# Optimization experiments

Measured on AMD Instinct MI355X. Metric: run time of the kernel, lower is better.

The kernel has to match this reference:

```python
import jax, jax.numpy as jnp
import numpy as np

# dims from VideoTokenizerConfig defaults + chosen video shape
B, T, IH, IW, C = 2, 16, 224, 224, 3
TP, PS, D, DFF, L, NH, K = 4, 16, 512, 2048, 6, 8, 8192
Tp, Hp, Wp = T // TP, IH // PS, IW // PS   # 4, 14, 14
S = Tp * Hp * Wp                           # 784 tokens
PIN = TP * PS * PS * C                     # 3072 patch elements
COMMIT = 0.25


def _ln(x, s, b):
    m = x.mean(-1, keepdims=True)
    v = ((x - m) ** 2).mean(-1, keepdims=True)
    return (x - m) / jnp.sqrt(v + 1e-6) * s + b


def _mha(x, Wqkv, bqkv, Wo, bo):
    b_, s_, d_ = x.shape
    hd = d_ // NH
    q = (x @ Wqkv[0] + bqkv[0]).reshape(b_, s_, NH, hd)
    k = (x @ Wqkv[1] + bqkv[1]).reshape(b_, s_, NH, hd)
    v = (x @ Wqkv[2] + bqkv[2]).reshape(b_, s_, NH, hd)
    att = jax.nn.softmax(jnp.einsum('bqhd,bkhd->bhqk', q, k) / jnp.sqrt(jnp.float32(hd)), axis=-1)
    o = jnp.einsum('bhqk,bkhd->bqhd', att, v).reshape(b_, s_, d_)
    return o @ Wo + bo


def _blocks(z, ln1s, ln1b, Wqkv, bqkv, Wo, bo, ln2s, ln2b, W1, b1, W2, b2):
    for i in range(L):  # small fixed layer count
        z = z + _mha(_ln(z, ln1s[i], ln1b[i]), Wqkv[i], bqkv[i], Wo[i], bo[i])
        h = jax.nn.gelu(_ln(z, ln2s[i], ln2b[i]) @ W1[i] + b1[i])
        z = z + h @ W2[i] + b2[i]
    return z


def _forward(video, e_patch_W, e_patch_b, e_pos_t, e_pos_h, e_pos_w,
             e_ln1_s, e_ln1_b, e_Wqkv, e_bqkv, e_Wo, e_bo, e_ln2_s, e_ln2_b,
             e_W1, e_b1, e_W2, e_b2, e_lnf_s, e_lnf_b, e_cb_W, e_cb_b,
             codebook,
             d_cb_W, d_cb_b, d_pos_t, d_pos_h, d_pos_w,
             d_ln1_s, d_ln1_b, d_Wqkv, d_bqkv, d_Wo, d_bo, d_ln2_s, d_ln2_b,
             d_W1, d_b1, d_W2, d_b2, d_lnf_s, d_lnf_b, d_px_W, d_px_b):
    # ---- encoder: 3D patchify ----
    v = video.reshape(B, Tp, TP, Hp, PS, Wp, PS, C)
    v = v.transpose(0, 1, 3, 5, 2, 4, 6, 7).reshape(B, Tp, Hp, Wp, PIN)
    z = v @ e_patch_W + e_patch_b
    z = z + e_pos_t + e_pos_h + e_pos_w
    z = z.reshape(B, S, D)
    z = _blocks(z, e_ln1_s, e_ln1_b, e_Wqkv, e_bqkv, e_Wo, e_bo,
                e_ln2_s, e_ln2_b, e_W1, e_b1, e_W2, e_b2)
    z = _ln(z, e_lnf_s, e_lnf_b)
    z_e = z @ e_cb_W + e_cb_b                      # [B,S,D]
    # ---- VQ quantize ----
    flat = z_e.reshape(-1, D)                      # [B*S, D]
    d2 = (flat ** 2).sum(1, keepdims=True) + (codebook ** 2).sum(1) - 2.0 * flat @ codebook.T
    idx = jnp.argmin(d2, axis=1)                   # [B*S]
    z_q = codebook[idx].reshape(z_e.shape)
    commit = jnp.mean((jax.lax.stop_gradient(z_q) - z_e) ** 2)
    cb_loss = jnp.mean((z_q - jax.lax.stop_gradient(z_e)) ** 2)
    z_q = z_e + jax.lax.stop_gradient(z_q - z_e)   # straight-through
    counts = jnp.zeros((K,), flat.dtype).at[idx].add(1.0)
    p = counts / idx.shape[0]                      # == mean(one_hot, axis=0)
    perplexity = jnp.exp(-jnp.sum(p * jnp.log(p + 1e-10)))
    # ---- decoder ----
    zd = z_q.reshape(B, Tp, Hp, Wp, D) @ d_cb_W + d_cb_b
    zd = zd + d_pos_t + d_pos_h + d_pos_w
    zd = zd.reshape(B, S, D)
    zd = _blocks(zd, d_ln1_s, d_ln1_b, d_Wqkv, d_bqkv, d_Wo, d_bo,
                 d_ln2_s, d_ln2_b, d_W1, d_b1, d_W2, d_b2)
    zd = _ln(zd, d_lnf_s, d_lnf_b)
    px = zd.reshape(B, Tp, Hp, Wp, D) @ d_px_W + d_px_b
    px = px.reshape(B, Tp, Hp, Wp, TP, PS, PS, C)
    recon = px.transpose(0, 1, 4, 2, 5, 3, 6, 7).reshape(B, T, IH, IW, C)
    return recon, idx.reshape(B, Tp, Hp, Wp), commit, cb_loss, perplexity


def setup_inputs() -> dict:
    key = jax.random.key(0)
    ks = iter(jax.random.split(key, 48))
    def nrm(shape, s=0.02):
        return (s * jax.random.normal(next(ks), shape)).astype(jnp.float32)
    z = lambda shape: jnp.zeros(shape, jnp.float32)
    o = lambda shape: jnp.ones(shape, jnp.float32)
    inp = {}
    inp['video'] = jax.random.normal(next(ks), (B, T, IH, IW, C), jnp.float32)
    # encoder params
    inp['e_patch_W'] = nrm((PIN, D)); inp['e_patch_b'] = z((D,))
    inp['e_pos_t'] = nrm((1, Tp, 1, 1, D)); inp['e_pos_h'] = nrm((1, 1, Hp, 1, D)); inp['e_pos_w'] = nrm((1, 1, 1, Wp, D))
    inp['e_ln1_s'] = o((L, D)); inp['e_ln1_b'] = z((L, D))
    inp['e_Wqkv'] = nrm((L, 3, D, D)); inp['e_bqkv'] = z((L, 3, D))
    inp['e_Wo'] = nrm((L, D, D)); inp['e_bo'] = z((L, D))
    inp['e_ln2_s'] = o((L, D)); inp['e_ln2_b'] = z((L, D))
    inp['e_W1'] = nrm((L, D, DFF)); inp['e_b1'] = z((L, DFF))
    inp['e_W2'] = nrm((L, DFF, D)); inp['e_b2'] = z((L, D))
    inp['e_lnf_s'] = o((D,)); inp['e_lnf_b'] = z((D,))
    inp['e_cb_W'] = nrm((D, D)); inp['e_cb_b'] = z((D,))
    inp['codebook'] = nrm((K, D))
    # decoder params
    inp['d_cb_W'] = nrm((D, D)); inp['d_cb_b'] = z((D,))
    inp['d_pos_t'] = nrm((1, Tp, 1, 1, D)); inp['d_pos_h'] = nrm((1, 1, Hp, 1, D)); inp['d_pos_w'] = nrm((1, 1, 1, Wp, D))
    inp['d_ln1_s'] = o((L, D)); inp['d_ln1_b'] = z((L, D))
    inp['d_Wqkv'] = nrm((L, 3, D, D)); inp['d_bqkv'] = z((L, 3, D))
    inp['d_Wo'] = nrm((L, D, D)); inp['d_bo'] = z((L, D))
    inp['d_ln2_s'] = o((L, D)); inp['d_ln2_b'] = z((L, D))
    inp['d_W1'] = nrm((L, D, DFF)); inp['d_b1'] = z((L, DFF))
    inp['d_W2'] = nrm((L, DFF, D)); inp['d_b2'] = z((L, D))
    inp['d_lnf_s'] = o((D,)); inp['d_lnf_b'] = z((D,))
    inp['d_px_W'] = nrm((D, PIN)); inp['d_px_b'] = z((PIN,))
    return inp


def reference(video, e_patch_W, e_patch_b, e_pos_t, e_pos_h, e_pos_w,
              e_ln1_s, e_ln1_b, e_Wqkv, e_bqkv, e_Wo, e_bo, e_ln2_s, e_ln2_b,
              e_W1, e_b1, e_W2, e_b2, e_lnf_s, e_lnf_b, e_cb_W, e_cb_b,
              codebook,
              d_cb_W, d_cb_b, d_pos_t, d_pos_h, d_pos_w,
              d_ln1_s, d_ln1_b, d_Wqkv, d_bqkv, d_Wo, d_bo, d_ln2_s, d_ln2_b,
              d_W1, d_b1, d_W2, d_b2, d_lnf_s, d_lnf_b, d_px_W, d_px_b):
    return _forward(video, e_patch_W, e_patch_b, e_pos_t, e_pos_h, e_pos_w,
                    e_ln1_s, e_ln1_b, e_Wqkv, e_bqkv, e_Wo, e_bo, e_ln2_s, e_ln2_b,
                    e_W1, e_b1, e_W2, e_b2, e_lnf_s, e_lnf_b, e_cb_W, e_cb_b,
                    codebook,
                    d_cb_W, d_cb_b, d_pos_t, d_pos_h, d_pos_w,
                    d_ln1_s, d_ln1_b, d_Wqkv, d_bqkv, d_Wo, d_bo, d_ln2_s, d_ln2_b,
                    d_W1, d_b1, d_W2, d_b2, d_lnf_s, d_lnf_b, d_px_W, d_px_b)
```

## Files before the change

### kernel.cpp

```cpp
#include <hip/hip_runtime.h>
#include <math.h>

#define Bq    2
#define Dq    512
#define DFFq  2048
#define Lq    6
#define NHq   8
#define HDq   64
#define Kq    8192
#define Sq    784
#define PINq  3072
#define TOKq  1568
#define RECN  4816896L

#define OFF_BIG  0L
#define SZ_BIG   12845056L
#define OFF_Z    (OFF_BIG + SZ_BIG)
#define OFF_XLN  (OFF_Z    + 802816L)
#define OFF_QKV  (OFF_XLN  + 802816L)
#define OFF_ATTO (OFF_QKV  + 2408448L)
#define OFF_H    (OFF_ATTO + 802816L)
#define OFF_ZE   (OFF_H    + 3211264L)
#define OFF_ZQ   (OFF_ZE   + 802816L)
#define OFF_CN   (OFF_ZQ   + 802816L)
#define OFF_IDX  (OFF_CN   + 8192L)
#define OFF_CNT  (OFF_IDX  + 1568L)
#define OFF_PART (OFF_CNT  + 8192L)
#define OFF_MIN  (OFF_PART + 1568L)
#define OFF_END  (OFF_MIN  + 3136L)

#define CEXT 802816L

typedef short bf16x8 __attribute__((ext_vector_type(8)));
typedef float f32x4  __attribute__((ext_vector_type(4)));
typedef unsigned short u16;
typedef unsigned long long u64;

#define XLO 802816L
#define QLO 2408448L
#define ALO 802816L
#define HLO 3211264L
#define PLO 4816896L
#define ZLO 802816L
#define CBLO 4194304L


__device__ __forceinline__ float wave_sum(float v) {
    #pragma unroll
    for (int o = 32; o; o >>= 1) v += __shfl_xor(v, o);
    return v;
}
__device__ __forceinline__ float gelu_f(float x) {
    float u = 0.7978845608028654f * (x + 0.044715f * x * x * x);
    float a = fabsf(u);
    float t = __expf(-2.0f * a);
    float th = (1.0f - t) / (1.0f + t);
    th = copysignf(th, u);
    return 0.5f * x * (1.0f + th);
}
__device__ __forceinline__ void split_f32(float x, u16& h, u16& l) {
    unsigned u = __float_as_uint(x);
    unsigned t = u + 0x7fffu + ((u >> 16) & 1u);
    h = (u16)(t >> 16);
    float r = x - __uint_as_float((t >> 16) << 16);
    l = (u16)(__float_as_uint(r) >> 16);
}
__device__ __forceinline__ void gload16(const u16* g, u16* l) {
    __builtin_amdgcn_global_load_lds(
        (const __attribute__((address_space(1))) void*)g,
        (__attribute__((address_space(3))) void*)l,
        16, 0, 0);
}

__global__ __launch_bounds__(256)
void wconv_t(const float* __restrict__ W, int ldw, int Kd,
             u16* __restrict__ WT, long loT, long soW, long soT)
{
    __shared__ u16 Lh[32][33], Ll[32][33];
    const float* Wp = W + (long)blockIdx.z * soW;
    u16* Tp = WT + (long)blockIdx.z * soT;
    int k0 = blockIdx.x << 5, n0 = blockIdx.y << 5;
    int t = threadIdx.x;
    int r = t >> 3, c4 = (t & 7) << 2;
    float4 v = *(const float4*)(Wp + (long)(k0 + r) * ldw + n0 + c4);
    u16 h, l;
    split_f32(v.x, h, l); Lh[c4+0][r] = h; Ll[c4+0][r] = l;
    split_f32(v.y, h, l); Lh[c4+1][r] = h; Ll[c4+1][r] = l;
    split_f32(v.z, h, l); Lh[c4+2][r] = h; Ll[c4+2][r] = l;
    split_f32(v.w, h, l); Lh[c4+3][r] = h; Ll[c4+3][r] = l;
    __syncthreads();
    int n = t >> 3, kc = (t & 7) << 2;
    u16* dst = Tp + (long)(n0 + n) * Kd + k0 + kc;
    u16 oh[4] = {Lh[n][kc], Lh[n][kc+1], Lh[n][kc+2], Lh[n][kc+3]};
    u16 ol[4] = {Ll[n][kc], Ll[n][kc+1], Ll[n][kc+2], Ll[n][kc+3]};
    *(uint2*)dst = *(uint2*)oh;
    *(uint2*)(dst + loT) = *(uint2*)ol;
}

// ... 13 lines not shown
    } else if (id < 1024) {
        int rid = id - 768; kblk = rid & 15; nblk = rid >> 4;
        W = Wo; ldw = 512; Kd = 512; Tp = dst + 1572864; loT = 262144;
    } else if (id < 2048) {
        int rid = id - 1024; kblk = rid & 15; nblk = rid >> 4;
        W = W1; ldw = 2048; Kd = 512; Tp = dst + 2097152; loT = 1048576;
    } else {
        int rid = id - 2048; kblk = rid & 63; nblk = rid >> 6;
        W = W2; ldw = 512; Kd = 2048; Tp = dst + 4194304; loT = 1048576;
    }
    int k0 = kblk << 5, n0 = nblk << 5;
    int t = threadIdx.x;
    int r = t >> 3, c4 = (t & 7) << 2;
    float4 v = *(const float4*)(W + (long)(k0 + r) * ldw + n0 + c4);
    u16 h, l;
    split_f32(v.x, h, l); Lh[c4+0][r] = h; Ll[c4+0][r] = l;
    split_f32(v.y, h, l); Lh[c4+1][r] = h; Ll[c4+1][r] = l;
    split_f32(v.z, h, l); Lh[c4+2][r] = h; Ll[c4+2][r] = l;
    split_f32(v.w, h, l); Lh[c4+3][r] = h; Ll[c4+3][r] = l;
    __syncthreads();
    int n = t >> 3, kc = (t & 7) << 2;
    u16* d = Tp + (long)(n0 + n) * Kd + k0 + kc;
    u16 oh[4] = {Lh[n][kc], Lh[n][kc+1], Lh[n][kc+2], Lh[n][kc+3]};
    u16 ol[4] = {Ll[n][kc], Ll[n][kc+1], Ll[n][kc+2], Ll[n][kc+3]};
    *(uint2*)d = *(uint2*)oh;
    *(uint2*)(d + loT) = *(uint2*)ol;
}

__global__ __launch_bounds__(256)
void splitp(const float* __restrict__ X, u16* __restrict__ Y, long lo, long n4)
{
    long i = (long)blockIdx.x * 256 + threadIdx.x;
    if (i >= n4) return;
    float4 v = *(const float4*)(X + i * 4);
    u16 h[4], l[4];
    split_f32(v.x, h[0], l[0]); split_f32(v.y, h[1], l[1]);
    split_f32(v.z, h[2], l[2]); split_f32(v.w, h[3], l[3]);
    *(uint2*)(Y + i * 4) = *(uint2*)h;
    *(uint2*)(Y + lo + i * 4) = *(uint2*)l;
}

template<int MATH, bool X2>
__global__ __launch_bounds__(256)
void gemm_bb(const u16* __restrict__ A, long rsA, long loA, long soA, long siA,
             const u16* __restrict__ B, long rsB, long loB, long soB, long siB,
             const float* __restrict__ bias, long siBias,
             const float* __restrict__ extra,
             float* __restrict__ Cf, int ldc, long soC, long siC,
             u16* __restrict__ Cb, int rsC, long loC,
             float* __restrict__ part, long pstride,
             int M, int N, int K, float alpha,
             int bdiv, int ksplit, int klen, int gx)
{
    __shared__ u16 Ah[2][2048], Al[2][2048], Bh[2][2048], Bl[2][2048];
    const int zb2 = blockIdx.z;
    const int zk = zb2 % ksplit, zb = zb2 / ksplit;
    const int zo = zb / bdiv, zi = zb - zo * bdiv;
    A += zo * soA + zi * siA;
    B += zo * soB + zi * siB;
    const float* bi = bias ? bias + zi * siBias : nullptr;

    const int nwg = gridDim.x;
    int orig = blockIdx.x;
    int qq = nwg >> 3, rr = nwg & 7;
    int xcd = orig & 7, sidx = orig >> 3;
    int wgid = (xcd < rr ? xcd * (qq + 1) : rr * (qq + 1) + (xcd - rr) * qq) + sidx;
    const int m0 = (wgid % gx) << 6, n0 = (wgid / gx) << 6;

    const int t = threadIdx.x;
    const int kbeg = zk * klen;
    int kend = kbeg + klen; if (kend > K) kend = K;

    const int w = t >> 6, lane = t & 63;
    const int wm = w >> 1, wn = w & 1;
    const int l15 = lane & 15, lk = (lane >> 4) << 3;
    const int wq = w << 9;

    int arow = m0 + (t >> 2); if (arow > M - 1) arow = M - 1;
    const u16* Apr = A + (long)arow * rsA + ((t & 3) << 3);
    const u16* Bpr = B + (long)(n0 + (t >> 2)) * rsB + ((t & 3) << 3);

    f32x4 acc[2][2] = {};

    for (int k0 = kbeg; k0 < kend; k0 += 64) {
        gload16(Apr + k0,            &Ah[0][wq]);
        gload16(Apr + k0 + loA,      &Al[0][wq]);
        gload16(Bpr + k0,            &Bh[0][wq]);
        if (!X2) gload16(Bpr + k0 + loB, &Bl[0][wq]);
        gload16(Apr + k0 + 32,       &Ah[1][wq]);
        gload16(Apr + k0 + 32 + loA, &Al[1][wq]);
        gload16(Bpr + k0 + 32,       &Bh[1][wq]);
        if (!X2) gload16(Bpr + k0 + 32 + loB, &Bl[1][wq]);
        __syncthreads();

        #pragma unroll
        for (int sub = 0; sub < 2; ++sub) {
            bf16x8 ah[2], al2[2], bh2[2], bl2[2];
            #pragma unroll
            for (int mi = 0; mi < 2; ++mi) {
                int row = (wm << 5) + (mi << 4) + l15;
                ah[mi]  = *(const bf16x8*)&Ah[sub][(row << 5) + lk];
                al2[mi] = *(const bf16x8*)&Al[sub][(row << 5) + lk];
            }
            #pragma unroll
            for (int ni = 0; ni < 2; ++ni) {
                int row = (wn << 5) + (ni << 4) + l15;
                bh2[ni] = *(const bf16x8*)&Bh[sub][(row << 5) + lk];
                if (!X2) bl2[ni] = *(const bf16x8*)&Bl[sub][(row << 5) + lk];
            }
            #pragma unroll
            for (int mi = 0; mi < 2; ++mi)
                #pragma unroll
                for (int ni = 0; ni < 2; ++ni) {
                    acc[mi][ni] = __builtin_amdgcn_mfma_f32_16x16x32_bf16(ah[mi], bh2[ni], acc[mi][ni], 0, 0, 0);
                    if (!X2) acc[mi][ni] = __builtin_amdgcn_mfma_f32_16x16x32_bf16(ah[mi], bl2[ni], acc[mi][ni], 0, 0, 0);
                    acc[mi][ni] = __builtin_amdgcn_mfma_f32_16x16x32_bf16(al2[mi], bh2[ni], acc[mi][ni], 0, 0, 0);
                }
        }
        __syncthreads();
    }

    if (ksplit > 1) {
        float* P = part + (long)zk * pstride + zo * soC + zi * siC;
        #pragma unroll
        for (int mi = 0; mi < 2; ++mi)
            #pragma unroll
            for (int ni = 0; ni < 2; ++ni) {
                int gn = n0 + (wn << 5) + (ni << 4) + l15;
                if (gn >= N) continue;
                int gmb = m0 + (wm << 5) + (mi << 4) + ((lane >> 4) << 2);
                #pragma unroll
                for (int r = 0; r < 4; ++r) {
                    int gm = gmb + r;
                    if (gm < M) P[(long)gm * ldc + gn] = acc[mi][ni][r];
                }
            }
        return;
    }
    if (MATH == 0) {
        float* Co = Cf + zo * soC + zi * siC;
        #pragma unroll
        for (int mi = 0; mi < 2; ++mi)
            #pragma unroll
            for (int ni = 0; ni < 2; ++ni) {
                int gn = n0 + (wn << 5) + (ni << 4) + l15;
                if (gn >= N) continue;
                int gmb = m0 + (wm << 5) + (mi << 4) + ((lane >> 4) << 2);
                #pragma unroll
                for (int r = 0; r < 4; ++r) {
                    int gm = gmb + r;
                    if (gm >= M) continue;
                    Co[(long)gm * ldc + gn] = alpha * acc[mi][ni][r] + (bi ? bi[gn] : 0.0f);
                }
            }
    } else if (MATH == 5) {
        u64* mb = (u64*)Cf;
        #pragma unroll
        for (int mi = 0; mi < 2; ++mi) {
            #pragma unroll
            for (int r = 0; r < 4; ++r) {
                u64 best = 0xFFFFFFFFFFFFFFFFULL;
                #pragma unroll
                for (int ni = 0; ni < 2; ++ni) {
                    int gn = n0 + (wn << 5) + (ni << 4) + l15;
                    float v = extra[gn] - 2.0f * acc[mi][ni][r];
                    unsigned ub = __float_as_uint(v);
                    ub = ub ^ ((ub >> 31) ? 0xFFFFFFFFu : 0x80000000u);
                    u64 pk = ((u64)ub << 32) | (unsigned)gn;
                    best = pk < best ? pk : best;
                }
                #pragma unroll
                for (int sft = 1; sft <= 8; sft <<= 1) {
                    u64 o = __shfl_xor(best, sft);
                    best = o < best ? o : best;
                }
                if (l15 == 0) {
                    int gm = m0 + (wm << 5) + (mi << 4) + ((lane >> 4) << 2) + r;
                    if (gm < M) atomicMin(&mb[gm], best);
                }
            }
        }
    } else {
        u16* Cu = Cb + zo * soC + zi * siC;
        #pragma unroll
        for (int mi = 0; mi < 2; ++mi)
            #pragma unroll
            for (int ni = 0; ni < 2; ++ni) {
                int gn = n0 + (wn << 5) + (ni << 4) + l15;
                if (gn >= N) continue;
                int gmb = m0 + (wm << 5) + (mi << 4) + ((lane >> 4) << 2);
                #pragma unroll
                for (int r = 0; r < 4; ++r) {
                    int gm = gmb + r;
                    if (gm >= M) continue;
                    float v = acc[mi][ni][r] + bi[gn];
                    u16 h, l; split_f32(v, h, l);
                    Cu[(long)gm * rsC + gn] = h;
                    Cu[(long)gm * rsC + gn + loC] = l;
                }
            }
    }
}

#define KP 72
#define VP 40
#define CHR 196
template<bool X2>
__global__ __launch_bounds__(256)
void flash_kernel(const u16* __restrict__ qkv, float* __restrict__ O4, float* __restrict__ ML)
{
    __shared__ u16 Kh[32 * KP], Kl[32 * KP];
    __shared__ u16 Vh[64 * VP], Vl[64 * VP];
    __shared__ u16 Ph[64 * VP], Pl[64 * VP];

    const int qb = blockIdx.x, bh = blockIdx.y, ch = blockIdx.z;
    const int b = bh >> 3, h = bh & 7;
    const int jbeg = ch * CHR, jend = jbeg + CHR;
    const int t = threadIdx.x, w = t >> 6, lane = t & 63;
    const int l15 = lane & 15, g = lane >> 4;
    const long base = (long)b * 784 * 1536;
    const u16* Qg = qkv + base + h * 64;
    const u16* Kg = qkv + base + 512 + h * 64;
    const u16* Vg = qkv + base + 1024 + h * 64;

    const int q0 = qb << 6;
    int qr = q0 + w * 16 + l15; if (qr > 783) qr = 783;
    const u16* Qp = Qg + (long)qr * 1536 + g * 8;
    bf16x8 qh[2], ql[2];
    qh[0] = *(const bf16x8*)(Qp);
    qh[1] = *(const bf16x8*)(Qp + 32);
    ql[0] = *(const bf16x8*)(Qp + QLO);
    ql[1] = *(const bf16x8*)(Qp + QLO + 32);

    f32x4 O[4] = {};
    float m_[4] = {-1e30f, -1e30f, -1e30f, -1e30f};
    float l_[4] = {};

    const int srow = t >> 3, sc = (t & 7) << 3;

    for (int j0 = jbeg; j0 < jend; j0 += 32) {
        {
            int jr = j0 + srow;
            if (jr < jend) {
                const u16* Kp = Kg + (long)jr * 1536 + sc;
                *(uint4*)&Kh[srow * KP + sc] = *(const uint4*)(Kp);
                if (!X2) *(uint4*)&Kl[srow * KP + sc] = *(const uint4*)(Kp + QLO);
                const u16* Vp = Vg + (long)jr * 1536 + sc;
                u16 th[8], tl[8];
                *(uint4*)th = *(const uint4*)Vp;
                if (!X2) *(uint4*)tl = *(const uint4*)(Vp + QLO);
                #pragma unroll
                for (int e = 0; e < 8; ++e) {
                    Vh[(sc + e) * VP + srow] = th[e];
                    if (!X2) Vl[(sc + e) * VP + srow] = tl[e];
                }
            } else {
                uint4 zz = {0, 0, 0, 0};
                *(uint4*)&Kh[srow * KP + sc] = zz;
                if (!X2) *(uint4*)&Kl[srow * KP + sc] = zz;
                #pragma unroll
                for (int e = 0; e < 8; ++e) {
                    Vh[(sc + e) * VP + srow] = 0;
                    if (!X2) Vl[(sc + e) * VP + srow] = 0;
                }
            }
        }
        __syncthreads();

        f32x4 S[2] = {};
        #pragma unroll
        for (int f = 0; f < 2; ++f) {
            #pragma unroll
            for (int ks = 0; ks < 2; ++ks) {
                bf16x8 kh = *(const bf16x8*)&Kh[(f * 16 + l15) * KP + ks * 32 + g * 8];
                S[f] = __builtin_amdgcn_mfma_f32_16x16x32_bf16(qh[ks], kh, S[f], 0, 0, 0);
                if (!X2) {
                    bf16x8 kl = *(const bf16x8*)&Kl[(f * 16 + l15) * KP + ks * 32 + g * 8];
                    S[f] = __builtin_amdgcn_mfma_f32_16x16x32_bf16(qh[ks], kl, S[f], 0, 0, 0);
                }
                S[f] = __builtin_amdgcn_mfma_f32_16x16x32_bf16(ql[ks], kh, S[f], 0, 0, 0);
            }
        }

        float p[2][4];
        #pragma unroll
        for (int f = 0; f < 2; ++f) {
            bool ok = (j0 + f * 16 + l15) < jend;
            #pragma unroll
            for (int r = 0; r < 4; ++r)
                p[f][r] = ok ? S[f][r] * 0.125f : -1e30f;
        }
        #pragma unroll
        for (int r = 0; r < 4; ++r) {
            float pm = fmaxf(p[0][r], p[1][r]);
            pm = fmaxf(pm, __shfl_xor(pm, 1)); pm = fmaxf(pm, __shfl_xor(pm, 2));
            pm = fmaxf(pm, __shfl_xor(pm, 4)); pm = fmaxf(pm, __shfl_xor(pm, 8));
            float mn = fmaxf(m_[r], pm);
            float scl = __expf(m_[r] - mn);
            float rs = 0.f;
            #pragma unroll
            for (int f = 0; f < 2; ++f) { float e = __expf(p[f][r] - mn); p[f][r] = e; rs += e; }
            rs += __shfl_xor(rs, 1); rs += __shfl_xor(rs, 2);
            rs += __shfl_xor(rs, 4); rs += __shfl_xor(rs, 8);
            l_[r] = l_[r] * scl + rs;
            m_[r] = mn;
            O[0][r] *= scl; O[1][r] *= scl; O[2][r] *= scl; O[3][r] *= scl;
        }

        #pragma unroll
        for (int f = 0; f < 2; ++f)
            #pragma unroll
            for (int r = 0; r < 4; ++r) {
                u16 hh, ll; split_f32(p[f][r], hh, ll);
                int row = w * 16 + g * 4 + r;
                Ph[row * VP + f * 16 + l15] = hh;
                Pl[row * VP + f * 16 + l15] = ll;
            }

        bf16x8 pah = *(const bf16x8*)&Ph[(w * 16 + l15) * VP + g * 8];
        bf16x8 pal = *(const bf16x8*)&Pl[(w * 16 + l15) * VP + g * 8];
        #pragma unroll
        for (int f = 0; f < 4; ++f) {
            bf16x8 vh = *(const bf16x8*)&Vh[(f * 16 + l15) * VP + g * 8];
            O[f] = __builtin_amdgcn_mfma_f32_16x16x32_bf16(pah, vh, O[f], 0, 0, 0);
            O[f] = __builtin_amdgcn_mfma_f32_16x16x32_bf16(pal, vh, O[f], 0, 0, 0);
            if (!X2) {
                bf16x8 vl = *(const bf16x8*)&Vl[(f * 16 + l15) * VP + g * 8];
                O[f] = __builtin_amdgcn_mfma_f32_16x16x32_bf16(pah, vl, O[f], 0, 0, 0);
            }
        }
        __syncthreads();
    }

    #pragma unroll
    for (int r = 0; r < 4; ++r) {
        int q = q0 + w * 16 + g * 4 + r;
        if (q >= 784) continue;
        long rowi = ((long)ch * 16 + bh) * 784 + q;
        if (l15 == 0) { ML[rowi * 2] = m_[r]; ML[rowi * 2 + 1] = l_[r]; }
        #pragma unroll
        for (int f = 0; f < 4; ++f)
            O4[rowi * 64 + f * 16 + l15] = O[f][r];
    }
}

__global__ __launch_bounds__(256)
void flash_combine(const float* __restrict__ O4, const float* __restrict__ ML,
                   u16* __restrict__ atto)
{
    int wave = threadIdx.x >> 6, lane = threadIdx.x & 63;
    int row = (blockIdx.x << 2) + wave;
    int bh = row / 784, q = row - bh * 784;
    int b = bh >> 3, h = bh & 7;
    float mm[4], ll[4];
    float M = -1e30f;
    #pragma unroll
    for (int c = 0; c < 4; ++c) {
        long ri = ((long)c * 16 + bh) * 784 + q;
        mm[c] = ML[ri * 2]; ll[c] = ML[ri * 2 + 1];
        M = fmaxf(M, mm[c]);
    }
    float L = 0.f, sc[4];
    #pragma unroll
    for (int c = 0; c < 4; ++c) { sc[c] = __expf(mm[c] - M); L += sc[c] * ll[c]; }
    float o = 0.f;
    #pragma unroll
    for (int c = 0; c < 4; ++c)
        o += O4[(((long)c * 16 + bh) * 784 + q) * 64 + lane] * sc[c];
    o /= L;
    u16 hh, lo2; split_f32(o, hh, lo2);
    long off = ((long)b * 784 + q) * 512 + h * 64 + lane;
    atto[off] = hh; atto[off + ALO] = lo2;
}

template<int MATH>
__global__ __launch_bounds__(256)
void reduce_k(const float* __restrict__ part, long pstride, int ks,
              const float* __restrict__ bias, int ldc,
              float* __restrict__ Cf, u16* __restrict__ Cb, long loC, long total)
{
    long i = (long)blockIdx.x * 256 + threadIdx.x;
    if (i >= total) return;
    float s = 0.f;
    for (int k = 0; k < ks; ++k) s += part[(long)k * pstride + i];
    int col = (int)(i % ldc);
    float v = s + (bias ? bias[col] : 0.0f);
    if (MATH == 3) { Cf[i] = v; u16 h, l; split_f32(v, h, l); Cb[i] = h; Cb[i + loC] = l; }
    else { float g = gelu_f(v); u16 h, l; split_f32(g, h, l); Cb[i] = h; Cb[i + loC] = l; }
}

__global__ __launch_bounds__(256)
void redln(const float* __restrict__ part, long pstride, int ks,
           const float* __restrict__ bias,
           float* __restrict__ z,
           const float* __restrict__ s, const float* __restrict__ b,
           u16* __restrict__ y, long lo)
{
    int wave = threadIdx.x >> 6, lane = threadIdx.x & 63;
    int row = (blockIdx.x << 2) + wave;
    int c0 = lane << 3;
    long base = (long)row * 512 + c0;
    float a[8] = {};
    for (int k = 0; k < ks; ++k) {
        const float* p = part + (long)k * pstride + base;
        float4 p0 = *(const float4*)p, p1 = *(const float4*)(p + 4);
        a[0]+=p0.x; a[1]+=p0.y; a[2]+=p0.z; a[3]+=p0.w;
        a[4]+=p1.x; a[5]+=p1.y; a[6]+=p1.z; a[7]+=p1.w;
    }
    float4 b0 = *(const float4*)(bias + c0), b1 = *(const float4*)(bias + c0 + 4);
    a[0]+=b0.x; a[1]+=b0.y; a[2]+=b0.z; a[3]+=b0.w;
    a[4]+=b1.x; a[5]+=b1.y; a[6]+=b1.z; a[7]+=b1.w;
    float4 z0 = *(const float4*)(z + base), z1 = *(const float4*)(z + base + 4);
    float v[8] = { z0.x+a[0], z0.y+a[1], z0.z+a[2], z0.w+a[3],
                   z1.x+a[4], z1.y+a[5], z1.z+a[6], z1.w+a[7] };
    float4 o0, o1;
    o0.x=v[0]; o0.y=v[1]; o0.z=v[2]; o0.w=v[3];
    o1.x=v[4]; o1.y=v[5]; o1.z=v[6]; o1.w=v[7];
    *(float4*)(z + base) = o0; *(float4*)(z + base + 4) = o1;
    float sum = v[0]+v[1]+v[2]+v[3]+v[4]+v[5]+v[6]+v[7];
    sum = wave_sum(sum);
    float m = sum * (1.0f / 512.0f);
    float var = 0.f;
    float d[8];
    #pragma unroll
    for (int j = 0; j < 8; ++j) { d[j] = v[j] - m; var += d[j]*d[j]; }
    var = wave_sum(var);
    float rstd = 1.0f / sqrtf(var * (1.0f / 512.0f) + 1e-6f);
    u16 hh[8], ll[8];
    #pragma unroll
    for (int j = 0; j < 8; ++j)
        split_f32(d[j] * rstd * s[c0+j] + b[c0+j], hh[j], ll[j]);
    *(uint4*)(y + base) = *(uint4*)hh;
    *(uint4*)(y + lo + base) = *(uint4*)ll;
}

__global__ __launch_bounds__(256)
void redposln(const float* __restrict__ part, long pstride, int ks,
              const float* __restrict__ bias,
              const float* __restrict__ pt, const float* __restrict__ ph,
              const float* __restrict__ pw,
// ... 104 lines not shown
        u16 h, l; split_f32(cv, h, l);
        zqp[(long)tok * Dq + d] = h;
        zqp[lo + (long)tok * Dq + d] = l;
        float df = cv - z[d];
        ss += df * df;
    }
    float wsum = wave_sum(ss);
    __shared__ float sw[4];
    if ((threadIdx.x & 63) == 0) sw[threadIdx.x >> 6] = wsum;
    __syncthreads();
    if (threadIdx.x == 0) {
        part[tok] = sw[0] + sw[1] + sw[2] + sw[3];
        atomicAdd(&counts[id], 1.0f);
        out_idx[tok] = (float)id;
    }
}

__global__ __launch_bounds__(256)
void scalars_kernel(const float* __restrict__ part, const float* __restrict__ counts,
                    float* __restrict__ out)
{
    float se = 0.f;
    for (int t = threadIdx.x; t < TOKq; t += 256) se += part[t];
    float pl = 0.f;
    for (int k = threadIdx.x; k < Kq; k += 256) {
        float p = counts[k] * (1.0f / 1568.0f);
        pl += p * logf(p + 1e-10f);
    }
    float wse = wave_sum(se), wpl = wave_sum(pl);
    __shared__ float s1[4], s2[4];
    if ((threadIdx.x & 63) == 0) { s1[threadIdx.x >> 6] = wse; s2[threadIdx.x >> 6] = wpl; }
    __syncthreads();
    if (threadIdx.x == 0) {
        float sse = s1[0] + s1[1] + s1[2] + s1[3];
        float plo = s2[0] + s2[1] + s2[2] + s2[3];
        float commit = sse / 802816.0f;
        out[RECN + 1568 + 0] = commit;
        out[RECN + 1568 + 1] = commit;
        out[RECN + 1568 + 2] = expf(-plo);
    }
}

template<bool X2>
static void block_fwd(hipStream_t st, float* z, float* big, float* hbuf,
                      u16* xlnu, u16* qkvu, u16* attou, u16* hbu, u16* wscr,
                      const float* Wqkv, const float* bqkv,
                      const float* Wo, const float* bo,
                      const float* ln2s, const float* ln2b,
                      const float* W1, const float* b1,
                      const float* W2, const float* b2,
                      const float* nls, const float* nlb)
{
    wconv4<<<3072, 256, 0, st>>>(Wqkv, Wo, W1, W2, wscr);
    gemm_bb<4, X2><<<dim3(600, 1, 1), 256, 0, st>>>(
        xlnu, Dq, XLO, 0, 0,
        wscr, Dq, 786432, 0, 0,
        bqkv, 0, nullptr,
        nullptr, 0, 0, 0,
        qkvu, 1536, QLO,
        nullptr, 0,
        TOKq, 1536, Dq, 1.0f, 1, 1, Dq, 25);
    flash_kernel<X2><<<dim3(13, 16, 4), 256, 0, st>>>(qkvu, big, big + 3211264L);
    flash_combine<<<3136, 256, 0, st>>>(big, big + 3211264L, attou);
    gemm_bb<0, X2><<<dim3(200, 1, 4), 256, 0, st>>>(
        attou, Dq, ALO, 0, 0,
        wscr + 1572864, Dq, 262144, 0, 0,
        nullptr, 0, nullptr,
        nullptr, Dq, 0, 0,
        nullptr, 0, 0,
        hbuf, CEXT,
        TOKq, Dq, Dq, 1.0f, 1, 4, 128, 25);
    redln<<<392, 256, 0, st>>>(hbuf, CEXT, 4, bo, z, ln2s, ln2b, xlnu, XLO);
    gemm_bb<0, X2><<<dim3(800, 1, 2), 256, 0, st>>>(
        xlnu, Dq, XLO, 0, 0,
        wscr + 2097152, Dq, 1048576, 0, 0,
        nullptr, 0, nullptr,
        nullptr, DFFq, 0, 0,
        nullptr, 0, 0,
        big, 3211264L,
        TOKq, DFFq, Dq, 1.0f, 1, 2, 256, 25);
    reduce_k<4><<<(3211264L + 255) / 256, 256, 0, st>>>(big, 3211264L, 2, b1, DFFq, nullptr, hbu, HLO, 3211264L);
    gemm_bb<0, X2><<<dim3(200, 1, 4), 256, 0, st>>>(
        hbu, DFFq, HLO, 0, 0,
        wscr + 4194304, DFFq, 1048576, 0, 0,
        nullptr, 0, nullptr,
        nullptr, Dq, 0, 0,
        nullptr, 0, 0,
        big, CEXT,
        TOKq, Dq, DFFq, 1.0f, 1, 4, 512, 25);
    redln<<<392, 256, 0, st>>>(big, CEXT, 4, b2, z, nls, nlb, xlnu, XLO);
}

extern "C" void kernel_launch(void* const* d_in, const int* in_sizes, int n_in,
                              void* d_out, int out_size, void* d_ws, size_t ws_size,
                              hipStream_t stream)
{
    (void)in_sizes; (void)n_in; (void)out_size;
    if (ws_size < (size_t)OFF_END * sizeof(float)) return;

    const float* video = (const float*)d_in[0];
    const float* epW   = (const float*)d_in[1];  const float* epb   = (const float*)d_in[2];
    const float* ept   = (const float*)d_in[3];  const float* ephp  = (const float*)d_in[4];
    const float* epwp  = (const float*)d_in[5];
    const float* eln1s = (const float*)d_in[6];  const float* eln1b = (const float*)d_in[7];
    const float* eWqkv = (const float*)d_in[8];  const float* ebqkv = (const float*)d_in[9];
    const float* eWo   = (const float*)d_in[10]; const float* ebo   = (const float*)d_in[11];
    const float* eln2s = (const float*)d_in[12]; const float* eln2b = (const float*)d_in[13];
    const float* eW1   = (const float*)d_in[14]; const float* eb1   = (const float*)d_in[15];
    const float* eW2   = (const float*)d_in[16]; const float* eb2   = (const float*)d_in[17];
    const float* elnfs = (const float*)d_in[18]; const float* elnfb = (const float*)d_in[19];
    const float* ecbW  = (const float*)d_in[20]; const float* ecbb  = (const float*)d_in[21];
    const float* cbook = (const float*)d_in[22];
    const float* dcbW  = (const float*)d_in[23]; const float* dcbb  = (const float*)d_in[24];
    const float* dpt   = (const float*)d_in[25]; const float* dphp  = (const float*)d_in[26];
    const float* dpwp  = (const float*)d_in[27];
    const float* dln1s = (const float*)d_in[28]; const float* dln1b = (const float*)d_in[29];
    const float* dWqkv = (const float*)d_in[30]; const float* dbqkv = (const float*)d_in[31];
    const float* dWo   = (const float*)d_in[32]; const float* dbo   = (const float*)d_in[33];
    const float* dln2s = (const float*)d_in[34]; const float* dln2b = (const float*)d_in[35];
    const float* dW1   = (const float*)d_in[36]; const float* db1   = (const float*)d_in[37];
    const float* dW2   = (const float*)d_in[38]; const float* db2   = (const float*)d_in[39];
    const float* dlnfs = (const float*)d_in[40]; const float* dlnfb = (const float*)d_in[41];
    const float* dpxW  = (const float*)d_in[42]; const float* dpxb  = (const float*)d_in[43];

    float* ws   = (float*)d_ws;
    float* big  = ws + OFF_BIG;
    float* z    = ws + OFF_Z;
    float* xln  = ws + OFF_XLN;
    float* qkv  = ws + OFF_QKV;
    float* atto = ws + OFF_ATTO;
    float* hbuf = ws + OFF_H;
    float* ze   = ws + OFF_ZE;
    float* zq   = ws + OFF_ZQ;
    float* cn   = ws + OFF_CN;
    float* cnt  = ws + OFF_CNT;
    float* part = ws + OFF_PART;
    u64*   minb = (u64*)(ws + OFF_MIN);
    float* out  = (float*)d_out;

    u16* xlnu  = (u16*)xln;
    u16* qkvu  = (u16*)qkv;
    u16* attou = (u16*)atto;
    u16* hbu   = (u16*)hbuf;
    u16* patu  = (u16*)big;
    u16* zqu   = (u16*)zq;
    u16* cbs   = (u16*)qkv;
    u16* wscr  = (u16*)(big + 9633792);

    hipMemsetAsync(cnt, 0, Kq * sizeof(float), stream);
    hipMemsetAsync(minb, 0xFF, TOKq * sizeof(u64), stream);
    cnorm_kernel<<<Kq / 4, 256, 0, stream>>>(cbook, cn);

    patchify_kernel<<<(int)(((long)TOKq * PINq + 255) / 256), 256, 0, stream>>>(video, patu);
    wconv_t<<<dim3(96, 16, 1), 256, 0, stream>>>(epW, Dq, PINq, wscr, 1572864, 0, 0);
    gemm_bb<0, false><<<dim3(200, 1, 6), 256, 0, stream>>>(
        patu, PINq, PLO, 0, 0,
        wscr, PINq, 1572864, 0, 0,
        nullptr, 0, nullptr,
        nullptr, Dq, 0, 0,
        nullptr, 0, 0,
        big + PLO, CEXT,
        TOKq, Dq, PINq, 1.0f, 1, 6, 512, 25);
    redposln<<<392, 256, 0, stream>>>(big + PLO, CEXT, 6, epb, ept, ephp, epwp,
                                      z, eln1s, eln1b, xlnu, XLO);

    for (int l = 0; l < Lq; ++l) {
        const float* nls = (l < 5) ? eln1s + (l + 1) * Dq : elnfs;
        const float* nlb = (l < 5) ? eln1b + (l + 1) * Dq : elnfb;
        block_fwd<false>(stream, z, big, hbuf, xlnu, qkvu, attou, hbu, wscr,
                         eWqkv + (long)l * 3 * Dq * Dq, ebqkv + l * 3 * Dq,
                         eWo + (long)l * Dq * Dq, ebo + l * Dq,
                         eln2s + l * Dq, eln2b + l * Dq,
                         eW1 + (long)l * Dq * DFFq, eb1 + l * DFFq,
                         eW2 + (long)l * DFFq * Dq, eb2 + l * Dq,
                         nls, nlb);
    }

    wconv_t<<<dim3(16, 16, 1), 256, 0, stream>>>(ecbW, Dq, Dq, wscr, 262144, 0, 0);
    gemm_bb<0, false><<<dim3(200, 1, 2), 256, 0, stream>>>(
        xlnu, Dq, XLO, 0, 0,
        wscr, Dq, 262144, 0, 0,
        nullptr, 0, nullptr,
        nullptr, Dq, 0, 0,
        nullptr, 0, 0,
        big, CEXT,
        TOKq, Dq, Dq, 1.0f, 1, 2, 256, 25);
    reduce_k<3><<<(CEXT + 255) / 256, 256, 0, stream>>>(big, CEXT, 2, ecbb, Dq, ze, zqu, ZLO, CEXT);

    splitp<<<(int)(((long)Kq * Dq / 4 + 255) / 256), 256, 0, stream>>>(cbook, cbs, CBLO, (long)Kq * Dq / 4);
    gemm_bb<5, false><<<dim3(3200, 1, 1), 256, 0, stream>>>(
        zqu, Dq, ZLO, 0, 0,
        cbs, Dq, CBLO, 0, 0,
        nullptr, 0, cn,
        (float*)minb, Kq, 0, 0,
        nullptr, 0, 0,
        nullptr, 0,
        TOKq, Kq, Dq, 1.0f, 1, 1, Dq, 25);
    zq_kernel<<<TOKq, 256, 0, stream>>>(cbook, minb, ze, zqu, ZLO, part, cnt, out + RECN);
    scalars_kernel<<<1, 256, 0, stream>>>(part, cnt, out);

    wconv_t<<<dim3(16, 16, 1), 256, 0, stream>>>(dcbW, Dq, Dq, wscr, 262144, 0, 0);
    gemm_bb<0, true><<<dim3(200, 1, 2), 256, 0, stream>>>(
        zqu, Dq, ZLO, 0, 0,
        wscr, Dq, 262144, 0, 0,
        nullptr, 0, nullptr,
        nullptr, Dq, 0, 0,
        nullptr, 0, 0,
        big, CEXT,
        TOKq, Dq, Dq, 1.0f, 1, 2, 256, 25);
    redposln<<<392, 256, 0, stream>>>(big, CEXT, 2, dcbb, dpt, dphp, dpwp,
                                      z, dln1s, dln1b, xlnu, XLO);

    for (int l = 0; l < Lq; ++l) {
        const float* nls = (l < 5) ? dln1s + (l + 1) * Dq : dlnfs;
        const float* nlb = (l < 5) ? dln1b + (l + 1) * Dq : dlnfb;
        block_fwd<true>(stream, z, big, hbuf, xlnu, qkvu, attou, hbu, wscr,
                        dWqkv + (long)l * 3 * Dq * Dq, dbqkv + l * 3 * Dq,
                        dWo + (long)l * Dq * Dq, dbo + l * Dq,
                        dln2s + l * Dq, dln2b + l * Dq,
                        dW1 + (long)l * Dq * DFFq, db1 + l * DFFq,
                        dW2 + (long)l * DFFq * Dq, db2 + l * Dq,
                        nls, nlb);
    }

    wconv_t<<<dim3(16, 96, 1), 256, 0, stream>>>(dpxW, PINq, Dq, wscr, 1572864, 0, 0);
    gemm_bb<0, true><<<dim3(1200, 1, 1), 256, 0, stream>>>(
        xlnu, Dq, XLO, 0, 0,
        wscr, Dq, 1572864, 0, 0,
        dpxb, 0, nullptr,
        big, PINq, 0, 0,
        nullptr, 0, 0,
        nullptr, 0,
        TOKq, PINq, Dq, 1.0f, 1, 1, Dq, 25);
    unpatchify_kernel<<<(int)((RECN + 255) / 256), 256, 0, stream>>>(big, out);
}
```

Before: 1.839 ms.

## Size shared memory per X2 variant and raise split-K/attention chunking

GEMM and flash kernels now use a single shared array sized by the X2 template, so the bf16x2 (X2) variants reserve less LDS and can fit more blocks per CU. Attention splits keys into 8 chunks instead of 4, and the combine step merges 8 partials. The QKV GEMM becomes split-K with a separate bias-reduce pass (new MATH==2), and several other GEMMs double their K-split. This raises parallelism on small GEMMs at the cost of extra partial-sum traffic and more reduction work.

```diff
diff --git a/kernel.cpp b/kernel.cpp
--- a/kernel.cpp
+++ b/kernel.cpp
@@ -43,7 +43,6 @@
 #define PLO 4816896L
 #define ZLO 802816L
 #define CBLO 4194304L
-
 
 __device__ __forceinline__ float wave_sum(float v) {
     #pragma unroll
@@ -163,7 +162,7 @@
              int M, int N, int K, float alpha,
              int bdiv, int ksplit, int klen, int gx)
 {
-    __shared__ u16 Ah[2][2048], Al[2][2048], Bh[2][2048], Bl[2][2048];
+    __shared__ u16 SH[X2 ? 12288 : 16384];
     const int zb2 = blockIdx.z;
     const int zk = zb2 % ksplit, zb = zb2 / ksplit;
     const int zo = zb / bdiv, zi = zb - zo * bdiv;
@@ -194,30 +193,31 @@
     f32x4 acc[2][2] = {};
 
     for (int k0 = kbeg; k0 < kend; k0 += 64) {
-        gload16(Apr + k0,            &Ah[0][wq]);
-        gload16(Apr + k0 + loA,      &Al[0][wq]);
-        gload16(Bpr + k0,            &Bh[0][wq]);
-        if (!X2) gload16(Bpr + k0 + loB, &Bl[0][wq]);
-        gload16(Apr + k0 + 32,       &Ah[1][wq]);
-        gload16(Apr + k0 + 32 + loA, &Al[1][wq]);
-        gload16(Bpr + k0 + 32,       &Bh[1][wq]);
-        if (!X2) gload16(Bpr + k0 + 32 + loB, &Bl[1][wq]);
+        gload16(Apr + k0,            &SH[wq]);
+        gload16(Apr + k0 + loA,      &SH[4096 + wq]);
+        gload16(Bpr + k0,            &SH[8192 + wq]);
+        if (!X2) gload16(Bpr + k0 + loB, &SH[12288 + wq]);
+        gload16(Apr + k0 + 32,       &SH[2048 + wq]);
+        gload16(Apr + k0 + 32 + loA, &SH[4096 + 2048 + wq]);
+        gload16(Bpr + k0 + 32,       &SH[8192 + 2048 + wq]);
+        if (!X2) gload16(Bpr + k0 + 32 + loB, &SH[12288 + 2048 + wq]);
         __syncthreads();
 
         #pragma unroll
         for (int sub = 0; sub < 2; ++sub) {
+            const int so = sub << 11;
             bf16x8 ah[2], al2[2], bh2[2], bl2[2];
             #pragma unroll
             for (int mi = 0; mi < 2; ++mi) {
                 int row = (wm << 5) + (mi << 4) + l15;
-                ah[mi]  = *(const bf16x8*)&Ah[sub][(row << 5) + lk];
-                al2[mi] = *(const bf16x8*)&Al[sub][(row << 5) + lk];
+                ah[mi]  = *(const bf16x8*)&SH[so + (row << 5) + lk];
+                al2[mi] = *(const bf16x8*)&SH[4096 + so + (row << 5) + lk];
             }
             #pragma unroll
             for (int ni = 0; ni < 2; ++ni) {
                 int row = (wn << 5) + (ni << 4) + l15;
-                bh2[ni] = *(const bf16x8*)&Bh[sub][(row << 5) + lk];
-                if (!X2) bl2[ni] = *(const bf16x8*)&Bl[sub][(row << 5) + lk];
+                bh2[ni] = *(const bf16x8*)&SH[8192 + so + (row << 5) + lk];
+                if (!X2) bl2[ni] = *(const bf16x8*)&SH[12288 + so + (row << 5) + lk];
             }
             #pragma unroll
             for (int mi = 0; mi < 2; ++mi)
@@ -315,14 +315,12 @@
 
 #define KP 72
 #define VP 40
-#define CHR 196
+#define CHR 98
 template<bool X2>
 __global__ __launch_bounds__(256)
 void flash_kernel(const u16* __restrict__ qkv, float* __restrict__ O4, float* __restrict__ ML)
 {
-    __shared__ u16 Kh[32 * KP], Kl[32 * KP];
-    __shared__ u16 Vh[64 * VP], Vl[64 * VP];
-    __shared__ u16 Ph[64 * VP], Pl[64 * VP];
+    __shared__ u16 SH[X2 ? 9984 : 14848];
 
     const int qb = blockIdx.x, bh = blockIdx.y, ch = blockIdx.z;
     const int b = bh >> 3, h = bh & 7;
@@ -354,25 +352,25 @@
             int jr = j0 + srow;
             if (jr < jend) {
                 const u16* Kp = Kg + (long)jr * 1536 + sc;
-                *(uint4*)&Kh[srow * KP + sc] = *(const uint4*)(Kp);
-                if (!X2) *(uint4*)&Kl[srow * KP + sc] = *(const uint4*)(Kp + QLO);
+                *(uint4*)&SH[srow * KP + sc] = *(const uint4*)(Kp);
+                if (!X2) *(uint4*)&SH[9984 + srow * KP + sc] = *(const uint4*)(Kp + QLO);
                 const u16* Vp = Vg + (long)jr * 1536 + sc;
                 u16 th[8], tl[8];
                 *(uint4*)th = *(const uint4*)Vp;
                 if (!X2) *(uint4*)tl = *(const uint4*)(Vp + QLO);
                 #pragma unroll
                 for (int e = 0; e < 8; ++e) {
-                    Vh[(sc + e) * VP + srow] = th[e];
-                    if (!X2) Vl[(sc + e) * VP + srow] = tl[e];
+                    SH[2304 + (sc + e) * VP + srow] = th[e];
+                    if (!X2) SH[12288 + (sc + e) * VP + srow] = tl[e];
                 }
             } else {
                 uint4 zz = {0, 0, 0, 0};
-                *(uint4*)&Kh[srow * KP + sc] = zz;
-                if (!X2) *(uint4*)&Kl[srow * KP + sc] = zz;
+                *(uint4*)&SH[srow * KP + sc] = zz;
+                if (!X2) *(uint4*)&SH[9984 + srow * KP + sc] = zz;
                 #pragma unroll
                 for (int e = 0; e < 8; ++e) {
-                    Vh[(sc + e) * VP + srow] = 0;
-                    if (!X2) Vl[(sc + e) * VP + srow] = 0;
+                    SH[2304 + (sc + e) * VP + srow] = 0;
+                    if (!X2) SH[12288 + (sc + e) * VP + srow] = 0;
                 }
             }
         }
@@ -383,10 +381,10 @@
         for (int f = 0; f < 2; ++f) {
             #pragma unroll
             for (int ks = 0; ks < 2; ++ks) {
-                bf16x8 kh = *(const bf16x8*)&Kh[(f * 16 + l15) * KP + ks * 32 + g * 8];
+                bf16x8 kh = *(const bf16x8*)&SH[(f * 16 + l15) * KP + ks * 32 + g * 8];
                 S[f] = __builtin_amdgcn_mfma_f32_16x16x32_bf16(qh[ks], kh, S[f], 0, 0, 0);
                 if (!X2) {
-                    bf16x8 kl = *(const bf16x8*)&Kl[(f * 16 + l15) * KP + ks * 32 + g * 8];
+                    bf16x8 kl = *(const bf16x8*)&SH[9984 + (f * 16 + l15) * KP + ks * 32 + g * 8];
                     S[f] = __builtin_amdgcn_mfma_f32_16x16x32_bf16(qh[ks], kl, S[f], 0, 0, 0);
                 }
                 S[f] = __builtin_amdgcn_mfma_f32_16x16x32_bf16(ql[ks], kh, S[f], 0, 0, 0);
@@ -424,19 +422,19 @@
             for (int r = 0; r < 4; ++r) {
                 u16 hh, ll; split_f32(p[f][r], hh, ll);
                 int row = w * 16 + g * 4 + r;
-                Ph[row * VP + f * 16 + l15] = hh;
-                Pl[row * VP + f * 16 + l15] = ll;
-            }
-
-        bf16x8 pah = *(const bf16x8*)&Ph[(w * 16 + l15) * VP + g * 8];
-        bf16x8 pal = *(const bf16x8*)&Pl[(w * 16 + l15) * VP + g * 8];
+                SH[4864 + row * VP + f * 16 + l15] = hh;
+                SH[7424 + row * VP + f * 16 + l15] = ll;
+            }
+
+        bf16x8 pah = *(const bf16x8*)&SH[4864 + (w * 16 + l15) * VP + g * 8];
+        bf16x8 pal = *(const bf16x8*)&SH[7424 + (w * 16 + l15) * VP + g * 8];
         #pragma unroll
         for (int f = 0; f < 4; ++f) {
-            bf16x8 vh = *(const bf16x8*)&Vh[(f * 16 + l15) * VP + g * 8];
+            bf16x8 vh = *(const bf16x8*)&SH[2304 + (f * 16 + l15) * VP + g * 8];
             O[f] = __builtin_amdgcn_mfma_f32_16x16x32_bf16(pah, vh, O[f], 0, 0, 0);
             O[f] = __builtin_amdgcn_mfma_f32_16x16x32_bf16(pal, vh, O[f], 0, 0, 0);
             if (!X2) {
-                bf16x8 vl = *(const bf16x8*)&Vl[(f * 16 + l15) * VP + g * 8];
+                bf16x8 vl = *(const bf16x8*)&SH[12288 + (f * 16 + l15) * VP + g * 8];
                 O[f] = __builtin_amdgcn_mfma_f32_16x16x32_bf16(pah, vl, O[f], 0, 0, 0);
             }
         }
@@ -463,20 +461,20 @@
     int row = (blockIdx.x << 2) + wave;
     int bh = row / 784, q = row - bh * 784;
     int b = bh >> 3, h = bh & 7;
-    float mm[4], ll[4];
+    float mm[8], ll[8];
     float M = -1e30f;
     #pragma unroll
-    for (int c = 0; c < 4; ++c) {
+    for (int c = 0; c < 8; ++c) {
         long ri = ((long)c * 16 + bh) * 784 + q;
         mm[c] = ML[ri * 2]; ll[c] = ML[ri * 2 + 1];
         M = fmaxf(M, mm[c]);
     }
-    float L = 0.f, sc[4];
-    #pragma unroll
-    for (int c = 0; c < 4; ++c) { sc[c] = __expf(mm[c] - M); L += sc[c] * ll[c]; }
+    float L = 0.f, sc[8];
+    #pragma unroll
+    for (int c = 0; c < 8; ++c) { sc[c] = __expf(mm[c] - M); L += sc[c] * ll[c]; }
     float o = 0.f;
     #pragma unroll
-    for (int c = 0; c < 4; ++c)
+    for (int c = 0; c < 8; ++c)
         o += O4[(((long)c * 16 + bh) * 784 + q) * 64 + lane] * sc[c];
     o /= L;
     u16 hh, lo2; split_f32(o, hh, lo2);
@@ -496,7 +494,8 @@
     for (int k = 0; k < ks; ++k) s += part[(long)k * pstride + i];
     int col = (int)(i % ldc);
     float v = s + (bias ? bias[col] : 0.0f);
-    if (MATH == 3) { Cf[i] = v; u16 h, l; split_f32(v, h, l); Cb[i] = h; Cb[i + loC] = l; }
+    if (MATH == 2) { u16 h, l; split_f32(v, h, l); Cb[i] = h; Cb[i + loC] = l; }
+    else if (MATH == 3) { Cf[i] = v; u16 h, l; split_f32(v, h, l); Cb[i] = h; Cb[i + loC] = l; }
     else { float g = gelu_f(v); u16 h, l; split_f32(g, h, l); Cb[i] = h; Cb[i + loC] = l; }
 }
 
@@ -707,25 +706,26 @@
                       const float* nls, const float* nlb)
 {
     wconv4<<<3072, 256, 0, st>>>(Wqkv, Wo, W1, W2, wscr);
-    gemm_bb<4, X2><<<dim3(600, 1, 1), 256, 0, st>>>(
+    gemm_bb<0, X2><<<dim3(600, 1, 2), 256, 0, st>>>(
         xlnu, Dq, XLO, 0, 0,
         wscr, Dq, 786432, 0, 0,
-        bqkv, 0, nullptr,
-        nullptr, 0, 0, 0,
-        qkvu, 1536, QLO,
-        nullptr, 0,
-        TOKq, 1536, Dq, 1.0f, 1, 1, Dq, 25);
-    flash_kernel<X2><<<dim3(13, 16, 4), 256, 0, st>>>(qkvu, big, big + 3211264L);
-    flash_combine<<<3136, 256, 0, st>>>(big, big + 3211264L, attou);
-    gemm_bb<0, X2><<<dim3(200, 1, 4), 256, 0, st>>>(
+        nullptr, 0, nullptr,
+        nullptr, 1536, 0, 0,
+        nullptr, 0, 0,
+        big, 2408448L,
+        TOKq, 1536, Dq, 1.0f, 1, 2, 256, 25);
+    reduce_k<2><<<(2408448L + 255) / 256, 256, 0, st>>>(big, 2408448L, 2, bqkv, 1536, nullptr, qkvu, QLO, 2408448L);
+    flash_kernel<X2><<<dim3(13, 16, 8), 256, 0, st>>>(qkvu, big, big + 6422528L);
+    flash_combine<<<3136, 256, 0, st>>>(big, big + 6422528L, attou);
+    gemm_bb<0, X2><<<dim3(200, 1, 8), 256, 0, st>>>(
         attou, Dq, ALO, 0, 0,
         wscr + 1572864, Dq, 262144, 0, 0,
         nullptr, 0, nullptr,
         nullptr, Dq, 0, 0,
         nullptr, 0, 0,
-        hbuf, CEXT,
-        TOKq, Dq, Dq, 1.0f, 1, 4, 128, 25);
-    redln<<<392, 256, 0, st>>>(hbuf, CEXT, 4, bo, z, ln2s, ln2b, xlnu, XLO);
+        big, CEXT,
+        TOKq, Dq, Dq, 1.0f, 1, 8, 64, 25);
+    redln<<<392, 256, 0, st>>>(big, CEXT, 8, bo, z, ln2s, ln2b, xlnu, XLO);
     gemm_bb<0, X2><<<dim3(800, 1, 2), 256, 0, st>>>(
         xlnu, Dq, XLO, 0, 0,
         wscr + 2097152, Dq, 1048576, 0, 0,
@@ -735,15 +735,15 @@
         big, 3211264L,
         TOKq, DFFq, Dq, 1.0f, 1, 2, 256, 25);
     reduce_k<4><<<(3211264L + 255) / 256, 256, 0, st>>>(big, 3211264L, 2, b1, DFFq, nullptr, hbu, HLO, 3211264L);
-    gemm_bb<0, X2><<<dim3(200, 1, 4), 256, 0, st>>>(
+    gemm_bb<0, X2><<<dim3(200, 1, 8), 256, 0, st>>>(
         hbu, DFFq, HLO, 0, 0,
         wscr + 4194304, DFFq, 1048576, 0, 0,
         nullptr, 0, nullptr,
         nullptr, Dq, 0, 0,
         nullptr, 0, 0,
         big, CEXT,
-        TOKq, Dq, DFFq, 1.0f, 1, 4, 512, 25);
-    redln<<<392, 256, 0, st>>>(big, CEXT, 4, b2, z, nls, nlb, xlnu, XLO);
+        TOKq, Dq, DFFq, 1.0f, 1, 8, 256, 25);
+    redln<<<392, 256, 0, st>>>(big, CEXT, 8, b2, z, nls, nlb, xlnu, XLO);
 }
 
 extern "C" void kernel_launch(void* const* d_in, const int* in_sizes, int n_in,
@@ -832,15 +832,15 @@
     }
 
     wconv_t<<<dim3(16, 16, 1), 256, 0, stream>>>(ecbW, Dq, Dq, wscr, 262144, 0, 0);
-    gemm_bb<0, false><<<dim3(200, 1, 2), 256, 0, stream>>>(
+    gemm_bb<0, false><<<dim3(200, 1, 4), 256, 0, stream>>>(
         xlnu, Dq, XLO, 0, 0,
         wscr, Dq, 262144, 0, 0,
         nullptr, 0, nullptr,
         nullptr, Dq, 0, 0,
         nullptr, 0, 0,
         big, CEXT,
-        TOKq, Dq, Dq, 1.0f, 1, 2, 256, 25);
-    reduce_k<3><<<(CEXT + 255) / 256, 256, 0, stream>>>(big, CEXT, 2, ecbb, Dq, ze, zqu, ZLO, CEXT);
+        TOKq, Dq, Dq, 1.0f, 1, 4, 128, 25);
+    reduce_k<3><<<(CEXT + 255) / 256, 256, 0, stream>>>(big, CEXT, 4, ecbb, Dq, ze, zqu, ZLO, CEXT);
 
     splitp<<<(int)(((long)Kq * Dq / 4 + 255) / 256), 256, 0, stream>>>(cbook, cbs, CBLO, (long)Kq * Dq / 4);
     gemm_bb<5, false><<<dim3(3200, 1, 1), 256, 0, stream>>>(
@@ -855,15 +855,15 @@
     scalars_kernel<<<1, 256, 0, stream>>>(part, cnt, out);
 
     wconv_t<<<dim3(16, 16, 1), 256, 0, stream>>>(dcbW, Dq, Dq, wscr, 262144, 0, 0);
-    gemm_bb<0, true><<<dim3(200, 1, 2), 256, 0, stream>>>(
+    gemm_bb<0, true><<<dim3(200, 1, 4), 256, 0, stream>>>(
         zqu, Dq, ZLO, 0, 0,
         wscr, Dq, 262144, 0, 0,
         nullptr, 0, nullptr,
         nullptr, Dq, 0, 0,
         nullptr, 0, 0,
         big, CEXT,
-        TOKq, Dq, Dq, 1.0f, 1, 2, 256, 25);
-    redposln<<<392, 256, 0, stream>>>(big, CEXT, 2, dcbb, dpt, dphp, dpwp,
+        TOKq, Dq, Dq, 1.0f, 1, 4, 128, 25);
+    redposln<<<392, 256, 0, stream>>>(big, CEXT, 4, dcbb, dpt, dphp, dpwp,
                                       z, dln1s, dln1b, xlnu, XLO);
 
     for (int l = 0; l < Lq; ++l) {
```

New measurement: 2.021 ms. 9.9% more time.

## Software-pipeline GEMM k-loop with double-buffered LDS and vmcnt waits

Applied to the files above, without the earlier changes.

Restructures the split-bf16 GEMM main loop to prefetch the next 32-wide k-slice into the alternate LDS buffer while computing the current one. It uses explicit s_waitcnt vmcnt and raw barriers so global-to-LDS loads overlap the MFMA work, followed by a separate epilogue iteration. It also shrinks the Bl shared buffer for the X2 variant, which lowers LDS use and may raise occupancy. The risks are hand-tuned waitcnt counts and fewer k elements per barrier.

```diff
diff --git a/kernel.cpp b/kernel.cpp
--- a/kernel.cpp
+++ b/kernel.cpp
@@ -43,7 +43,6 @@
 #define PLO 4816896L
 #define ZLO 802816L
 #define CBLO 4194304L
-
 
 __device__ __forceinline__ float wave_sum(float v) {
     #pragma unroll
@@ -163,7 +162,8 @@
              int M, int N, int K, float alpha,
              int bdiv, int ksplit, int klen, int gx)
 {
-    __shared__ u16 Ah[2][2048], Al[2][2048], Bh[2][2048], Bl[2][2048];
+    __shared__ u16 Ah[2][2048], Al[2][2048], Bh[2][2048];
+    __shared__ u16 Bl[X2 ? 2 : 2][X2 ? 64 : 2048];
     const int zb2 = blockIdx.z;
     const int zk = zb2 % ksplit, zb = zb2 / ksplit;
     const int zo = zb / bdiv, zi = zb - zo * bdiv;
@@ -193,31 +193,39 @@
 
     f32x4 acc[2][2] = {};
 
-    for (int k0 = kbeg; k0 < kend; k0 += 64) {
-        gload16(Apr + k0,            &Ah[0][wq]);
-        gload16(Apr + k0 + loA,      &Al[0][wq]);
-        gload16(Bpr + k0,            &Bh[0][wq]);
-        if (!X2) gload16(Bpr + k0 + loB, &Bl[0][wq]);
-        gload16(Apr + k0 + 32,       &Ah[1][wq]);
-        gload16(Apr + k0 + 32 + loA, &Al[1][wq]);
-        gload16(Bpr + k0 + 32,       &Bh[1][wq]);
-        if (!X2) gload16(Bpr + k0 + 32 + loB, &Bl[1][wq]);
-        __syncthreads();
-
-        #pragma unroll
-        for (int sub = 0; sub < 2; ++sub) {
+    const int nk = (kend - kbeg) >> 5;
+    gload16(Apr + kbeg,       &Ah[0][wq]);
+    gload16(Apr + kbeg + loA, &Al[0][wq]);
+    gload16(Bpr + kbeg,       &Bh[0][wq]);
+    if (!X2) gload16(Bpr + kbeg + loB, &Bl[0][wq]);
+
+    int i = 0;
+    for (; i + 1 < nk; ++i) {
+        asm volatile("" ::: "memory");
+        const int nb = (i + 1) & 1;
+        const int ka = kbeg + ((i + 1) << 5);
+        gload16(Apr + ka,       &Ah[nb][wq]);
+        gload16(Apr + ka + loA, &Al[nb][wq]);
+        gload16(Bpr + ka,       &Bh[nb][wq]);
+        if (!X2) gload16(Bpr + ka + loB, &Bl[nb][wq]);
+        if (X2) asm volatile("s_waitcnt vmcnt(3)" ::: "memory");
+        else    asm volatile("s_waitcnt vmcnt(4)" ::: "memory");
+        __builtin_amdgcn_s_barrier();
+        asm volatile("" ::: "memory");
+        {
+            const int cb = i & 1;
             bf16x8 ah[2], al2[2], bh2[2], bl2[2];
             #pragma unroll
             for (int mi = 0; mi < 2; ++mi) {
                 int row = (wm << 5) + (mi << 4) + l15;
-                ah[mi]  = *(const bf16x8*)&Ah[sub][(row << 5) + lk];
-                al2[mi] = *(const bf16x8*)&Al[sub][(row << 5) + lk];
+                ah[mi]  = *(const bf16x8*)&Ah[cb][(row << 5) + lk];
+                al2[mi] = *(const bf16x8*)&Al[cb][(row << 5) + lk];
             }
             #pragma unroll
             for (int ni = 0; ni < 2; ++ni) {
                 int row = (wn << 5) + (ni << 4) + l15;
-                bh2[ni] = *(const bf16x8*)&Bh[sub][(row << 5) + lk];
-                if (!X2) bl2[ni] = *(const bf16x8*)&Bl[sub][(row << 5) + lk];
+                bh2[ni] = *(const bf16x8*)&Bh[cb][(row << 5) + lk];
+                if (!X2) bl2[ni] = *(const bf16x8*)&Bl[cb][(row << 5) + lk];
             }
             #pragma unroll
             for (int mi = 0; mi < 2; ++mi)
@@ -228,7 +236,33 @@
                     acc[mi][ni] = __builtin_amdgcn_mfma_f32_16x16x32_bf16(al2[mi], bh2[ni], acc[mi][ni], 0, 0, 0);
                 }
         }
-        __syncthreads();
+        asm volatile("" ::: "memory");
+        __builtin_amdgcn_s_barrier();
+    }
+    __syncthreads();
+    {
+        const int cb = i & 1;
+        bf16x8 ah[2], al2[2], bh2[2], bl2[2];
+        #pragma unroll
+        for (int mi = 0; mi < 2; ++mi) {
+            int row = (wm << 5) + (mi << 4) + l15;
+            ah[mi]  = *(const bf16x8*)&Ah[cb][(row << 5) + lk];
+            al2[mi] = *(const bf16x8*)&Al[cb][(row << 5) + lk];
+        }
+        #pragma unroll
+        for (int ni = 0; ni < 2; ++ni) {
+            int row = (wn << 5) + (ni << 4) + l15;
+            bh2[ni] = *(const bf16x8*)&Bh[cb][(row << 5) + lk];
+            if (!X2) bl2[ni] = *(const bf16x8*)&Bl[cb][(row << 5) + lk];
+        }
+        #pragma unroll
+        for (int mi = 0; mi < 2; ++mi)
+            #pragma unroll
+            for (int ni = 0; ni < 2; ++ni) {
+                acc[mi][ni] = __builtin_amdgcn_mfma_f32_16x16x32_bf16(ah[mi], bh2[ni], acc[mi][ni], 0, 0, 0);
+                if (!X2) acc[mi][ni] = __builtin_amdgcn_mfma_f32_16x16x32_bf16(ah[mi], bl2[ni], acc[mi][ni], 0, 0, 0);
+                acc[mi][ni] = __builtin_amdgcn_mfma_f32_16x16x32_bf16(al2[mi], bh2[ni], acc[mi][ni], 0, 0, 0);
+            }
     }
 
     if (ksplit > 1) {
```

Result: slower. 1.887 ms (+2.6%).
